# Kernel optimization log

Measured on AMD Instinct MI355X. Metric: run time of the kernel, lower is better.

## Reference

```python
import jax, jax.numpy as jnp
import numpy as np

VOCAB = 100000
NUM_SENSES = 8
VEC_DIM = 128
BATCH = 16384
CTX = 10  # context words -> x has 2 + CTX columns


def setup_inputs() -> dict:
    key = jax.random.key(0)
    kx, kg, ks = jax.random.split(key, 3)
    x = jax.random.randint(kx, (BATCH, 2 + CTX), 0, VOCAB, dtype=jnp.int32)
    W_g = jax.random.normal(kg, (VOCAB, VEC_DIM), dtype=jnp.float32) * 0.1
    W_s = jax.random.normal(ks, (VOCAB, NUM_SENSES, VEC_DIM), dtype=jnp.float32) * 0.1
    return {"x": x, "W_g": W_g, "W_s": W_s}


def reference(x, W_g, W_s):
    # sum of global vectors of the context words: [B, D]
    sum_context = jnp.sum(W_g[x[:, 2:]], axis=1)
    # sense vectors of the target word: [B, K, D]
    sense_vecs = W_s[x[:, 0]]
    # per-sense score against the context: [B, K]
    scores = jnp.einsum("bkd,bd->bk", sense_vecs, sum_context)
    # route to best sense per example: [B]
    right_senses = jnp.argmax(scores, axis=1)
    # gather the chosen sense vector: [B, D]
    chosen = jnp.take_along_axis(sense_vecs, right_senses[:, None, None], axis=1)[:, 0, :]
    # dot with the global vector of the second word -> [B, 1], sigmoid activation
    dot_prod = jnp.einsum("bd,bd->b", chosen, W_g[x[:, 1]])[:, None]
    return jax.nn.sigmoid(dot_prod)
```

## Files before the change

### kernel.cpp

```cpp
#include <hip/hip_runtime.h>
#include <hip/hip_bf16.h>
#include <cmath>

#define BATCH     16384
#define CTX       10
#define NSENSE    8
#define VEC_DIM   128
#define XCOLS     (2 + CTX)

__global__ __launch_bounds__(256) void SenseEmbedding_40295383171457_kernel(
    const int*   __restrict__ x,
    const float* __restrict__ Wg,
    const float* __restrict__ Ws,
    float*       __restrict__ out)
{
    const int gtid = blockIdx.x * blockDim.x + threadIdx.x;
    const int elem = gtid >> 4;
    const int sub  = gtid & 15;
    if (elem >= BATCH) return;

    const int4* xr4 = reinterpret_cast<const int4*>(x + elem * XCOLS);
    const int4 xa = xr4[0];
    const int4 xb = xr4[1];
    const int4 xc = xr4[2];
    const int off = sub * 8;

    const float* tgt = Wg + (size_t)xa.y * VEC_DIM + off;
    const float4 t0 = *reinterpret_cast<const float4*>(tgt);
    const float4 t1 = *reinterpret_cast<const float4*>(tgt + 4);

    const int cidx[CTX] = {xa.z, xa.w, xb.x, xb.y, xb.z, xb.w,
                           xc.x, xc.y, xc.z, xc.w};
    float4 c0 = make_float4(0.f, 0.f, 0.f, 0.f);
    float4 c1 = make_float4(0.f, 0.f, 0.f, 0.f);
    #pragma unroll
    for (int c = 0; c < CTX; ++c) {
        const float* row = Wg + (size_t)cidx[c] * VEC_DIM + off;
        const float4 a = *reinterpret_cast<const float4*>(row);
        const float4 b = *reinterpret_cast<const float4*>(row + 4);
        c0.x += a.x; c0.y += a.y; c0.z += a.z; c0.w += a.w;
        c1.x += b.x; c1.y += b.y; c1.z += b.z; c1.w += b.w;
    }

    const float* srow = Ws + (size_t)xa.x * (NSENSE * VEC_DIM);
    float p[NSENSE], q[NSENSE];
    #pragma unroll
    for (int k = 0; k < NSENSE; ++k) {
        const float* r = srow + k * VEC_DIM + off;
        const float4 a = *reinterpret_cast<const float4*>(r);
        const float4 b = *reinterpret_cast<const float4*>(r + 4);
        p[k] = a.x * c0.x + a.y * c0.y + a.z * c0.z + a.w * c0.w
             + b.x * c1.x + b.y * c1.y + b.z * c1.z + b.w * c1.w;
        q[k] = a.x * t0.x + a.y * t0.y + a.z * t0.z + a.w * t0.w
             + b.x * t1.x + b.y * t1.y + b.z * t1.z + b.w * t1.w;
    }

    #pragma unroll
    for (int k = 0; k < NSENSE; ++k) {
        float v = p[k];
        #pragma unroll
        for (int s = 8; s > 0; s >>= 1)
            v += __shfl_xor(v, s, 16);
        p[k] = v;
    }

    int   best = 0;
    float bv   = p[0];
    #pragma unroll
    for (int k = 1; k < NSENSE; ++k) {
        if (p[k] > bv) { bv = p[k]; best = k; }
    }

    float qb = q[0];
    #pragma unroll
    for (int k = 1; k < NSENSE; ++k)
        qb = (best == k) ? q[k] : qb;
    #pragma unroll
    for (int s = 8; s > 0; s >>= 1)
        qb += __shfl_xor(qb, s, 16);

    if (sub == 0) {
        out[elem] = 1.f / (1.f + expf(-qb));
    }
}

extern "C" void kernel_launch(void* const* d_in, const int* in_sizes, int n_in,
                              void* d_out, int out_size, void* d_ws, size_t ws_size,
                              hipStream_t stream) {
    const int*   x  = (const int*)  d_in[0];
    const float* Wg = (const float*)d_in[1];
    const float* Ws = (const float*)d_in[2];
    float*       out = (float*)d_out;

    const int elems_per_block = 256 / 16;
    const int grid = (BATCH + elems_per_block - 1) / elems_per_block;
    SenseEmbedding_40295383171457_kernel<<<grid, 256, 0, stream>>>(x, Wg, Ws, out);
}
```

Measured before the change: 486.0 us.

## Use 32 lanes per example with one float4 each and nontemporal sense loads

Each batch element now gets 32 threads instead of 16, so every lane loads a single float4 per row rather than two, and the grid doubles. Sense-vector loads use nontemporal hints because those rows are not reused, and index math switches to 32-bit unsigned. The aim is more memory-level parallelism and more waves in flight for a latency-bound gather. The cost is an extra shuffle-reduction step per sense and redundant index loads across twice as many threads.

```diff
diff --git a/kernel.cpp b/kernel.cpp
--- a/kernel.cpp
+++ b/kernel.cpp
@@ -1,5 +1,4 @@
 #include <hip/hip_runtime.h>
-#include <hip/hip_bf16.h>
 #include <cmath>
 
 #define BATCH     16384
@@ -8,6 +7,8 @@
 #define VEC_DIM   128
 #define XCOLS     (2 + CTX)
 
+typedef float f4 __attribute__((ext_vector_type(4)));
+
 __global__ __launch_bounds__(256) void SenseEmbedding_40295383171457_kernel(
     const int*   __restrict__ x,
     const float* __restrict__ Wg,
@@ -15,52 +16,45 @@
     float*       __restrict__ out)
 {
     const int gtid = blockIdx.x * blockDim.x + threadIdx.x;
-    const int elem = gtid >> 4;
-    const int sub  = gtid & 15;
+    const int elem = gtid >> 5;
+    const int sub  = gtid & 31;
     if (elem >= BATCH) return;
 
     const int4* xr4 = reinterpret_cast<const int4*>(x + elem * XCOLS);
     const int4 xa = xr4[0];
     const int4 xb = xr4[1];
     const int4 xc = xr4[2];
-    const int off = sub * 8;
+    const int off = sub * 4;
 
-    const float* tgt = Wg + (size_t)xa.y * VEC_DIM + off;
-    const float4 t0 = *reinterpret_cast<const float4*>(tgt);
-    const float4 t1 = *reinterpret_cast<const float4*>(tgt + 4);
+    const f4 t = *reinterpret_cast<const f4*>(
+        Wg + (unsigned)xa.y * VEC_DIM + off);
 
     const int cidx[CTX] = {xa.z, xa.w, xb.x, xb.y, xb.z, xb.w,
                            xc.x, xc.y, xc.z, xc.w};
-    float4 c0 = make_float4(0.f, 0.f, 0.f, 0.f);
-    float4 c1 = make_float4(0.f, 0.f, 0.f, 0.f);
+    f4 c = {0.f, 0.f, 0.f, 0.f};
     #pragma unroll
-    for (int c = 0; c < CTX; ++c) {
-        const float* row = Wg + (size_t)cidx[c] * VEC_DIM + off;
-        const float4 a = *reinterpret_cast<const float4*>(row);
-        const float4 b = *reinterpret_cast<const float4*>(row + 4);
-        c0.x += a.x; c0.y += a.y; c0.z += a.z; c0.w += a.w;
-        c1.x += b.x; c1.y += b.y; c1.z += b.z; c1.w += b.w;
+    for (int i = 0; i < CTX; ++i) {
+        const f4 a = *reinterpret_cast<const f4*>(
+            Wg + (unsigned)cidx[i] * VEC_DIM + off);
+        c += a;
     }
 
-    const float* srow = Ws + (size_t)xa.x * (NSENSE * VEC_DIM);
+    const float* srow = Ws + (unsigned)xa.x * (NSENSE * VEC_DIM) + off;
     float p[NSENSE], q[NSENSE];
     #pragma unroll
     for (int k = 0; k < NSENSE; ++k) {
-        const float* r = srow + k * VEC_DIM + off;
-        const float4 a = *reinterpret_cast<const float4*>(r);
-        const float4 b = *reinterpret_cast<const float4*>(r + 4);
-        p[k] = a.x * c0.x + a.y * c0.y + a.z * c0.z + a.w * c0.w
-             + b.x * c1.x + b.y * c1.y + b.z * c1.z + b.w * c1.w;
-        q[k] = a.x * t0.x + a.y * t0.y + a.z * t0.z + a.w * t0.w
-             + b.x * t1.x + b.y * t1.y + b.z * t1.z + b.w * t1.w;
+        const f4 a = __builtin_nontemporal_load(
+            reinterpret_cast<const f4*>(srow + k * VEC_DIM));
+        p[k] = a.x * c.x + a.y * c.y + a.z * c.z + a.w * c.w;
+        q[k] = a.x * t.x + a.y * t.y + a.z * t.z + a.w * t.w;
     }
 
     #pragma unroll
     for (int k = 0; k < NSENSE; ++k) {
         float v = p[k];
         #pragma unroll
-        for (int s = 8; s > 0; s >>= 1)
-            v += __shfl_xor(v, s, 16);
+        for (int s = 16; s > 0; s >>= 1)
+            v += __shfl_xor(v, s, 32);
         p[k] = v;
     }
 
@@ -76,8 +70,8 @@
     for (int k = 1; k < NSENSE; ++k)
         qb = (best == k) ? q[k] : qb;
     #pragma unroll
-    for (int s = 8; s > 0; s >>= 1)
-        qb += __shfl_xor(qb, s, 16);
+    for (int s = 16; s > 0; s >>= 1)
+        qb += __shfl_xor(qb, s, 32);
 
     if (sub == 0) {
         out[elem] = 1.f / (1.f + expf(-qb));
@@ -92,7 +86,7 @@
     const float* Ws = (const float*)d_in[2];
     float*       out = (float*)d_out;
 
-    const int elems_per_block = 256 / 16;
+    const int elems_per_block = 256 / 32;
     const int grid = (BATCH + elems_per_block - 1) / elems_per_block;
     SenseEmbedding_40295383171457_kernel<<<grid, 256, 0, stream>>>(x, Wg, Ws, out);
 }
```

Result: no change. 482.4 us (-0.8%).
